# Kernel optimization log

Hardware: AMD Instinct MI355X
Metric: run time of the kernel (lower is better)

Reference implementation:

```python
import jax, jax.numpy as jnp
import numpy as np

THETA = 128.0


def _make_Q(d, units):
    # Q[n,m] = (2n+1)/sqrt(d) if n > m and (n+m) odd, else 0 (fixed, non-trainable)
    n = np.arange(d)[:, None]
    m = np.arange(units)[None, :]
    Q = np.where((n > m) & (((n + m) % 2) == 1), (2 * n + 1) / np.sqrt(d), 0.0)
    return jnp.asarray(Q, dtype=jnp.float32)


def setup_inputs() -> dict:
    key = jax.random.key(0)
    k1, k2, k3, k4 = jax.random.split(key, 4)
    B_, T, Din, d, units = 16, 4096, 128, 256, 256
    x = jax.random.normal(k1, (B_, T, Din), dtype=jnp.float32)
    A = jax.random.normal(k2, (d, d), dtype=jnp.float32) / np.sqrt(d)
    Bm = jax.random.normal(k3, (Din, d), dtype=jnp.float32) / np.sqrt(Din)
    W_mix = jax.random.normal(k4, (units, units), dtype=jnp.float32) / np.sqrt(units)
    b_mix = jnp.zeros((units,), dtype=jnp.float32)
    return {"x": x, "A": A, "B": Bm, "W_mix": W_mix, "b_mix": b_mix}


def reference(x, A, B, W_mix, b_mix):
    d = A.shape[0]
    units = W_mix.shape[0]
    Q = _make_Q(d, units)
    QW = Q @ W_mix  # fuse fixed projection with dense kernel: (d, units)
    alpha = 1.0 - 1.0 / THETA
    beta = 1.0 / THETA
    # precompute input projection for all steps: (T, batch, d)
    xB = jnp.einsum('bti,id->tbd', x, B)

    def step(state, xBt):
        new_state = alpha * state + beta * (state @ A + xBt)
        y = jnp.tanh(new_state @ QW + b_mix)
        return new_state, y

    s0 = jnp.zeros((x.shape[0], d), dtype=x.dtype)
    _, ys = jax.lax.scan(step, s0, xB)  # ys: (T, batch, units)
    return jnp.transpose(ys, (1, 0, 2))
```

## Files before the change

### kernel.cpp

```cpp
#include <hip/hip_runtime.h>
#include <math.h>

constexpr int T_   = 4096;
constexpr int NB   = 16;
constexpr int D_   = 256;
constexpr int DIN  = 128;
constexpr int U_   = 256;
constexpr int L1   = 8;
constexpr int C1   = T_ / L1;
constexpr float ALPHA_ = 1.0f - 1.0f / 128.0f;
constexpr float BETA_  = 1.0f / 128.0f;
constexpr int SD   = NB * D_;
constexpr int MS   = D_ * D_;
constexpr int TLP  = D_ + 4;
constexpr int XLP  = DIN + 4;

using short8  = __attribute__((ext_vector_type(8))) short;
using float4v = __attribute__((ext_vector_type(4))) float;

__device__ __forceinline__ unsigned short bf16_rne(float x) {
  const unsigned b = __float_as_uint(x);
  const unsigned r = ((b >> 16) & 1u) + 0x7FFFu;
  return (unsigned short)((b + r) >> 16);
}
__device__ __forceinline__ float bf16_f(unsigned short h) {
  return __uint_as_float(((unsigned)h) << 16);
}

__device__ __forceinline__ void split2(float e0, float e1, unsigned& hd, unsigned& ld) {
  const unsigned b0 = __float_as_uint(e0), b1 = __float_as_uint(e1);
  const unsigned h0 = b0 & 0xFFFF0000u, h1 = b1 & 0xFFFF0000u;
  const float l0 = e0 - __uint_as_float(h0);
  const float l1 = e1 - __uint_as_float(h1);
  hd = (h0 >> 16) | h1;
  ld = (__float_as_uint(l0) >> 16) | (__float_as_uint(l1) & 0xFFFF0000u);
}

__device__ __forceinline__ void unpack8(uint4 a, uint4 b, short8& hi, short8& lo) {
  union { short8 s; unsigned u[4]; } H, L;
  const unsigned d[8] = {a.x, a.y, a.z, a.w, b.x, b.y, b.z, b.w};
#pragma unroll
  for (int i = 0; i < 4; ++i) {
    H.u[i] = (d[2 * i] >> 16) | (d[2 * i + 1] & 0xFFFF0000u);
    L.u[i] = (d[2 * i] & 0xFFFFu) | (d[2 * i + 1] << 16);
  }
  hi = H.s; lo = L.s;
}

__device__ __forceinline__ void mm_row(const float* __restrict__ Am,
                                       const float* __restrict__ Bm,
                                       float* __restrict__ Dm,
                                       int i, int tid, float* srow) {
  srow[tid] = Am[i * D_ + tid];
  __syncthreads();
  float a0 = 0.f, a1 = 0.f, a2 = 0.f, a3 = 0.f;
#pragma unroll 8
  for (int k = 0; k < D_; k += 4) {
    a0 = fmaf(srow[k + 0], Bm[(k + 0) * D_ + tid], a0);
    a1 = fmaf(srow[k + 1], Bm[(k + 1) * D_ + tid], a1);
    a2 = fmaf(srow[k + 2], Bm[(k + 2) * D_ + tid], a2);
    a3 = fmaf(srow[k + 3], Bm[(k + 3) * D_ + tid], a3);
  }
  Dm[i * D_ + tid] = (a0 + a1) + (a2 + a3);
  __syncthreads();
}

__global__ __launch_bounds__(256) void k_prep(const float* __restrict__ A,
                                              const float* __restrict__ W,
                                              float* __restrict__ Meff,
                                              float* __restrict__ QW) {
  const int bid = blockIdx.x, tid = threadIdx.x;
  if (bid < D_) {
    float v = BETA_ * A[bid * D_ + tid];
    if (bid == tid) v += ALPHA_;
    Meff[bid * D_ + tid] = v;
    return;
  }
  __shared__ float wch[32 * D_];
  float se = 0.f, so = 0.f;
  for (int ch = 0; ch < D_ / 32; ++ch) {
    __syncthreads();
    for (int idx = tid; idx < 32 * D_; idx += 256)
      wch[idx] = W[ch * 32 * D_ + idx];
    __syncthreads();
#pragma unroll
    for (int r = 0; r < 32; ++r) {
      const int n = ch * 32 + r;
      const float sum = (n & 1) ? se : so;
      QW[n * U_ + tid] = sum * ((float)(2 * n + 1) / 16.0f);
      const float wv = wch[r * D_ + tid];
      if (n & 1) so += wv; else se += wv;
    }
  }
}

__global__ __launch_bounds__(256) void k_pw(const float* __restrict__ Am,
                                            const float* __restrict__ Bbase,
                                            float* __restrict__ Dbase) {
  __shared__ float srow[D_];
  const int q = blockIdx.x >> 8, row = blockIdx.x & 255;
  mm_row(Am, Bbase + (size_t)q * MS, Dbase + (size_t)q * MS, row, threadIdx.x, srow);
}

__global__ __launch_bounds__(256) void k_pwr(const float* __restrict__ Abase,
                                             const float* __restrict__ Bm,
                                             float* __restrict__ Dbase) {
  __shared__ float srow[D_];
  const int q = blockIdx.x >> 8, row = blockIdx.x & 255;
  mm_row(Abase + (size_t)q * MS, Bm, Dbase + (size_t)q * MS, row, threadIdx.x, srow);
}

__global__ __launch_bounds__(256) void k_packA(const float* __restrict__ A,
                                               const float* __restrict__ Bm,
                                               unsigned short* __restrict__ Mf,
                                               unsigned short* __restrict__ Bmf) {
  const int bid = blockIdx.x, tid = threadIdx.x;
  const int lane = tid & 63, nb0 = tid >> 6;
  const int quad = lane >> 4, m16 = lane & 15;
  if (bid < 8) {
    const int ks = bid;
    for (int nb = nb0; nb < 16; nb += 4) {
      const size_t fo = ((size_t)(nb * 8 + ks) * 64 + lane) * 8;
#pragma unroll
      for (int jj = 0; jj < 8; ++jj) {
        const int k = ks * 32 + quad * 8 + jj;
        const int n = nb * 16 + m16;
        const float v = BETA_ * A[k * D_ + n];
        const unsigned short h = bf16_rne(v);
        Mf[fo + jj] = h;
        Mf[MS + fo + jj] = bf16_rne(v - bf16_f(h));
      }
    }
  } else {
    const int ks = bid - 8;
    unsigned short* dh = Bmf;
    unsigned short* dl = Bmf + (MS / 2);
    for (int nb = nb0; nb < 16; nb += 4) {
      const size_t fo = ((size_t)(nb * 4 + ks) * 64 + lane) * 8;
#pragma unroll
      for (int jj = 0; jj < 8; ++jj) {
        const int k = ks * 32 + quad * 8 + jj;
        const int n = nb * 16 + m16;
        const float v = BETA_ * Bm[k * D_ + n];
        const unsigned short h = bf16_rne(v);
        dh[fo + jj] = h;
        dl[fo + jj] = bf16_rne(v - bf16_f(h));
      }
    }
  }
}

__global__ __launch_bounds__(256) void k_packB(const float* __restrict__ R,
                                               const float* __restrict__ QWm,
                                               const float* __restrict__ M8,
                                               unsigned short* __restrict__ Bf,
                                               unsigned short* __restrict__ Pf0) {
  const int bid = blockIdx.x;
  const int mat = bid >> 3, ks = bid & 7;
  const float* X = (mat < 8) ? (R + (size_t)mat * MS) : (mat == 8 ? QWm : M8);
  unsigned short* dh = (mat < 9) ? (Bf + (size_t)mat * (2 * MS)) : Pf0;
  unsigned short* dl = dh + MS;
  const int tid = threadIdx.x, lane = tid & 63, nb0 = tid >> 6;
  const int quad = lane >> 4, m16 = lane & 15;
  for (int nb = nb0; nb < 16; nb += 4) {
    const size_t fo = ((size_t)(nb * 8 + ks) * 64 + lane) * 8;
#pragma unroll
    for (int jj = 0; jj < 8; ++jj) {
      const int k = ks * 32 + quad * 8 + jj;
      const int n = nb * 16 + m16;
      const float xv = X[k * D_ + n];
      const unsigned short h = bf16_rne(xv);
      dh[fo + jj] = h;
      dl[fo + jj] = bf16_rne(xv - bf16_f(h));
    }
  }
}

__global__ __launch_bounds__(256, 2) void k_passA(
    const float* __restrict__ x, const unsigned short* __restrict__ Bmf,
    const unsigned short* __restrict__ Mf,
    unsigned short* __restrict__ Shi, unsigned short* __restrict__ Slo,
    float* __restrict__ Ends) {
  __shared__ __align__(16) float xls[NB][XLP];
  __shared__ __align__(16) unsigned tls[NB][TLP];
  const int c = blockIdx.x, tid = threadIdx.x;
  const int w = tid >> 6, lane = tid & 63;
  const int m16 = lane & 15, q = lane >> 4;
  const int xrow = tid >> 4, xi0 = (tid & 15) * 8;

  float4v sC[4];
#pragma unroll
  for (int nt = 0; nt < 4; ++nt) sC[nt] = (float4v){0.f, 0.f, 0.f, 0.f};

  for (int j = 0; j < L1; ++j) {
    const int t = c * L1 + j;
    __syncthreads();
    {
      const float* xr = x + ((size_t)xrow * T_ + t) * DIN + xi0;
      const float4 v0 = *(const float4*)(xr);
      const float4 v1 = *(const float4*)(xr + 4);
      *(float4*)(&xls[xrow][xi0]) = v0;
      *(float4*)(&xls[xrow][xi0 + 4]) = v1;
    }
    if (j > 0) {
#pragma unroll
      for (int nt = 0; nt < 4; ++nt) {
        const int n = (w * 4 + nt) * 16 + m16;
#pragma unroll
        for (int r = 0; r < 4; ++r) {
          const float sv = sC[nt][r];
          const unsigned hb = __float_as_uint(sv) & 0xFFFF0000u;
          const float lo = sv - __uint_as_float(hb);
          tls[4 * q + r][n] = hb | (__float_as_uint(lo) >> 16);
        }
      }
    }
    __syncthreads();
    float4v acc[4];
#pragma unroll
    for (int nt = 0; nt < 4; ++nt) {
      acc[nt][0] = ALPHA_ * sC[nt][0];
      acc[nt][1] = ALPHA_ * sC[nt][1];
      acc[nt][2] = ALPHA_ * sC[nt][2];
      acc[nt][3] = ALPHA_ * sC[nt][3];
    }
#pragma unroll
    for (int ks = 0; ks < 4; ++ks) {
      float xv[8];
      *(float4*)(xv)     = *(const float4*)(&xls[m16][32 * ks + 8 * q]);
      *(float4*)(xv + 4) = *(const float4*)(&xls[m16][32 * ks + 8 * q + 4]);
      union { short8 s; unsigned u[4]; } XH, XL;
#pragma unroll
      for (int p = 0; p < 4; ++p) split2(xv[2 * p], xv[2 * p + 1], XH.u[p], XL.u[p]);
#pragma unroll
      for (int nt = 0; nt < 4; ++nt) {
        const size_t fo = ((size_t)((w * 4 + nt) * 4 + ks) * 64 + lane) * 8;
        const short8 bh = *(const short8*)(Bmf + fo);
        const short8 bl = *(const short8*)(Bmf + (MS / 2) + fo);
        acc[nt] = __builtin_amdgcn_mfma_f32_16x16x32_bf16(XH.s, bh, acc[nt], 0, 0, 0);
        acc[nt] = __builtin_amdgcn_mfma_f32_16x16x32_bf16(XH.s, bl, acc[nt], 0, 0, 0);
        acc[nt] = __builtin_amdgcn_mfma_f32_16x16x32_bf16(XL.s, bh, acc[nt], 0, 0, 0);
      }
    }
    if (j > 0) {
#pragma unroll
      for (int ks = 0; ks < 8; ++ks) {
        const uint4 p0 = *(const uint4*)(&tls[m16][32 * ks + 8 * q]);
        const uint4 p1 = *(const uint4*)(&tls[m16][32 * ks + 8 * q + 4]);
        short8 sh, sl; unpack8(p0, p1, sh, sl);
        const size_t ao = ((size_t)((t - 1) * 8 + ks) * 64 + lane) * 8;
        *(short8*)(Shi + ao) = sh;
        *(short8*)(Slo + ao) = sl;
#pragma unroll
        for (int nt = 0; nt < 4; ++nt) {
          const size_t fo = ((size_t)((w * 4 + nt) * 8 + ks) * 64 + lane) * 8;
          const short8 mh = *(const short8*)(Mf + fo);
          const short8 ml = *(const short8*)(Mf + MS + fo);
          acc[nt] = __builtin_amdgcn_mfma_f32_16x16x32_bf16(sh, mh, acc[nt], 0, 0, 0);
          acc[nt] = __builtin_amdgcn_mfma_f32_16x16x32_bf16(sh, ml, acc[nt], 0, 0, 0);
          acc[nt] = __builtin_amdgcn_mfma_f32_16x16x32_bf16(sl, mh, acc[nt], 0, 0, 0);
        }
      }
    }
#pragma unroll
    for (int nt = 0; nt < 4; ++nt) sC[nt] = acc[nt];
  }
  const int tl = c * L1 + L1 - 1;
  __syncthreads();
#pragma unroll
  for (int nt = 0; nt < 4; ++nt) {
    const int n = (w * 4 + nt) * 16 + m16;
#pragma unroll
    for (int r = 0; r < 4; ++r) {
      const float sv = sC[nt][r];
      const unsigned hb = __float_as_uint(sv) & 0xFFFF0000u;
      const float lo = sv - __uint_as_float(hb);
      tls[4 * q + r][n] = hb | (__float_as_uint(lo) >> 16);
    }
  }
  __syncthreads();
#pragma unroll
  for (int ks = 0; ks < 8; ++ks) {
    const uint4 p0 = *(const uint4*)(&tls[m16][32 * ks + 8 * q]);
    const uint4 p1 = *(const uint4*)(&tls[m16][32 * ks + 8 * q + 4]);
    short8 sh, sl; unpack8(p0, p1, sh, sl);
    const size_t ao = ((size_t)(tl * 8 + ks) * 64 + lane) * 8;
    *(short8*)(Shi + ao) = sh;
    *(short8*)(Slo + ao) = sl;
  }
#pragma unroll
  for (int nt = 0; nt < 4; ++nt) {
    const int n = (w * 4 + nt) * 16 + m16;
#pragma unroll
    for (int r = 0; r < 4; ++r)
      Ends[(size_t)c * SD + (size_t)(4 * q + r) * D_ + n] = sC[nt][r];
  }
}

__global__ __launch_bounds__(256) void k_scan(
    const float* __restrict__ Vin, float* __restrict__ Vout,
    const unsigned short* __restrict__ Pf,
    const float* __restrict__ Pf32,
    float* __restrict__ Psq,
    unsigned short* __restrict__ PfNext,
    int shift, int do_sq, int packmode,
    unsigned short* __restrict__ Hhi, unsigned short* __restrict__ Hlo) {
  __shared__ __align__(16) float smem[16 * TLP];
  const int bid = blockIdx.x, tid = threadIdx.x;
  if (bid >= C1) {
    if (!do_sq) return;
    const int i = bid - C1;
    smem[tid] = Pf32[i * D_ + tid];
    __syncthreads();
    float a0 = 0.f, a1 = 0.f, a2 = 0.f, a3 = 0.f;
#pragma unroll 8
    for (int k = 0; k < D_; k += 4) {
      a0 = fmaf(smem[k + 0], Pf32[(k + 0) * D_ + tid], a0);
      a1 = fmaf(smem[k + 1], Pf32[(k + 1) * D_ + tid], a1);
      a2 = fmaf(smem[k + 2], Pf32[(k + 2) * D_ + tid], a2);
      a3 = fmaf(smem[k + 3], Pf32[(k + 3) * D_ + tid], a3);
    }
    const float v = (a0 + a1) + (a2 + a3);
    Psq[i * D_ + tid] = v;
    const unsigned short h = bf16_rne(v);
    const unsigned short l = bf16_rne(v - bf16_f(h));
    const size_t off = ((size_t)((tid >> 4) * 8 + (i >> 5)) * 64 +
                        ((i >> 3) & 3) * 16 + (tid & 15)) * 8 + (i & 7);
    PfNext[off] = h;
    PfNext[MS + off] = l;
    return;
  }
  const int c = bid;
  const int w = tid >> 6, lane = tid & 63;
  const int m16 = lane & 15, q = lane >> 4;
  float4v acc[4];
#pragma unroll
  for (int nt = 0; nt < 4; ++nt) {
    const int n = (w * 4 + nt) * 16 + m16;
#pragma unroll
    for (int r = 0; r < 4; ++r)
      acc[nt][r] = Vin[(size_t)c * SD + (size_t)(4 * q + r) * D_ + n];
  }
  if (c >= shift) {
    const float* src = Vin + (size_t)(c - shift) * SD;
    {
      const int row = tid >> 4, col0 = (tid & 15) * 16;
#pragma unroll
      for (int p = 0; p < 4; ++p)
        *(float4*)(&smem[row * TLP + col0 + 4 * p]) =
            *(const float4*)(src + (size_t)row * D_ + col0 + 4 * p);
    }
    __syncthreads();
#pragma unroll
    for (int ks = 0; ks < 8; ++ks) {
      float xv[8];
      *(float4*)(xv)     = *(const float4*)(&smem[m16 * TLP + 32 * ks + 8 * q]);
      *(float4*)(xv + 4) = *(const float4*)(&smem[m16 * TLP + 32 * ks + 8 * q + 4]);
      union { short8 s; unsigned u[4]; } XH, XL;
#pragma unroll
      for (int p = 0; p < 4; ++p) split2(xv[2 * p], xv[2 * p + 1], XH.u[p], XL.u[p]);
#pragma unroll
      for (int nt = 0; nt < 4; ++nt) {
        const size_t fo = ((size_t)((w * 4 + nt) * 8 + ks) * 64 + lane) * 8;
        const short8 ph = *(const short8*)(Pf + fo);
        const short8 pl = *(const short8*)(Pf + MS + fo);
        acc[nt] = __builtin_amdgcn_mfma_f32_16x16x32_bf16(XH.s, ph, acc[nt], 0, 0, 0);
        acc[nt] = __builtin_amdgcn_mfma_f32_16x16x32_bf16(XH.s, pl, acc[nt], 0, 0, 0);
        acc[nt] = __builtin_amdgcn_mfma_f32_16x16x32_bf16(XL.s, ph, acc[nt], 0, 0, 0);
      }
    }
  }
  if (packmode) {
    __syncthreads();
    unsigned* tls = (unsigned*)smem;
#pragma unroll
    for (int nt = 0; nt < 4; ++nt) {
      const int n = (w * 4 + nt) * 16 + m16;
#pragma unroll
      for (int r = 0; r < 4; ++r) {
        const float sv = acc[nt][r];
        const unsigned hb = __float_as_uint(sv) & 0xFFFF0000u;
        const float lo = sv - __uint_as_float(hb);
        tls[(4 * q + r) * TLP + n] = hb | (__float_as_uint(lo) >> 16);
      }
    }
    __syncthreads();
#pragma unroll
    for (int ks = 0; ks < 8; ++ks) {
      const uint4 p0 = *(const uint4*)(&tls[m16 * TLP + 32 * ks + 8 * q]);
      const uint4 p1 = *(const uint4*)(&tls[m16 * TLP + 32 * ks + 8 * q + 4]);
      short8 sh, sl; unpack8(p0, p1, sh, sl);
      const size_t ao = ((size_t)(c * 8 + ks) * 64 + lane) * 8;
      *(short8*)(Hhi + ao) = sh;
      *(short8*)(Hlo + ao) = sl;
    }
  } else {
#pragma unroll
    for (int nt = 0; nt < 4; ++nt) {
      const int n = (w * 4 + nt) * 16 + m16;
#pragma unroll
      for (int r = 0; r < 4; ++r)
        Vout[(size_t)c * SD + (size_t)(4 * q + r) * D_ + n] = acc[nt][r];
    }
  }
}

__global__ __launch_bounds__(256, 3) void k_passB(
    const unsigned short* __restrict__ Shi, const unsigned short* __restrict__ Slo,
    const unsigned short* __restrict__ Hhi, const unsigned short* __restrict__ Hlo,
    const unsigned short* __restrict__ Bf, const float* __restrict__ bmix,
    float* __restrict__ out) {
  const int bid = blockIdx.x;
  const int g4 = (bid >> 3) * 4, j = bid & 7;
  const int tid = threadIdx.x;
  const int w = tid >> 6, lane = tid & 63;
  const int m16 = lane & 15, quad = lane >> 4;
  const unsigned short* Qh = Bf + (size_t)8 * 2 * MS;
  const unsigned short* Ql = Qh + MS;
  const unsigned short* Rh = Bf + (size_t)j * 2 * MS;
  const unsigned short* Rl = Rh + MS;

  float4v acc[4][4];
#pragma unroll
  for (int ci = 0; ci < 4; ++ci)
#pragma unroll
    for (int nt = 0; nt < 4; ++nt) acc[ci][nt] = (float4v){0.f, 0.f, 0.f, 0.f};

  for (int ks = 0; ks < 8; ++ks) {
    short8 fh[4], fl[4];
#pragma unroll
    for (int nt = 0; nt < 4; ++nt) {
      const size_t fo = ((size_t)((w * 4 + nt) * 8 + ks) * 64 + lane) * 8;
      fh[nt] = *(const short8*)(Qh + fo);
      fl[nt] = *(const short8*)(Ql + fo);
    }
#pragma unroll
    for (int ci = 0; ci < 4; ++ci) {
      const int t = (g4 + ci) * 8 + j;
      const size_t ao = ((size_t)(t * 8 + ks) * 64 + lane) * 8;
      const short8 sh = *(const short8*)(Shi + ao);
      const short8 sl = *(const short8*)(Slo + ao);
#pragma unroll
      for (int nt = 0; nt < 4; ++nt) {
        float4v a = acc[ci][nt];
        a = __builtin_amdgcn_mfma_f32_16x16x32_bf16(sh, fh[nt], a, 0, 0, 0);
        a = __builtin_amdgcn_mfma_f32_16x16x32_bf16(sh, fl[nt], a, 0, 0, 0);
        a = __builtin_amdgcn_mfma_f32_16x16x32_bf16(sl, fh[nt], a, 0, 0, 0);
        acc[ci][nt] = a;
      }
    }
#pragma unroll
    for (int nt = 0; nt < 4; ++nt) {
      const size_t fo = ((size_t)((w * 4 + nt) * 8 + ks) * 64 + lane) * 8;
      fh[nt] = *(const short8*)(Rh + fo);
      fl[nt] = *(const short8*)(Rl + fo);
    }
#pragma unroll
    for (int ci = 0; ci < 4; ++ci) {
      const int c = g4 + ci;
      if (c > 0) {
        const size_t ho = ((size_t)((c - 1) * 8 + ks) * 64 + lane) * 8;
        const short8 hh = *(const short8*)(Hhi + ho);
        const short8 hl = *(const short8*)(Hlo + ho);
#pragma unroll
        for (int nt = 0; nt < 4; ++nt) {
          float4v a = acc[ci][nt];
          a = __builtin_amdgcn_mfma_f32_16x16x32_bf16(hh, fh[nt], a, 0, 0, 0);
          a = __builtin_amdgcn_mfma_f32_16x16x32_bf16(hh, fl[nt], a, 0, 0, 0);
          a = __builtin_amdgcn_mfma_f32_16x16x32_bf16(hl, fh[nt], a, 0, 0, 0);
          acc[ci][nt] = a;
        }
      }
    }
  }
  __shared__ float ysm[16][U_ + 4];
  for (int ci = 0; ci < 4; ++ci) {
    const int t = (g4 + ci) * 8 + j;
    __syncthreads();
#pragma unroll
    for (int nt = 0; nt < 4; ++nt) {
      const int n = (w * 4 + nt) * 16 + m16;
      const float bias = bmix[n];
#pragma unroll
      for (int r = 0; r < 4; ++r) {
        const float v = acc[ci][nt][r] + bias;
        const float e = __expf(2.0f * v);
        ysm[quad * 4 + r][n] = 1.0f - 2.0f / (e + 1.0f);
      }
    }
    __syncthreads();
    for (int idx = tid; idx < 16 * (U_ / 4); idx += 256) {
      const int b = idx >> 6, c4 = (idx & 63) * 4;
      const float4 v = make_float4(ysm[b][c4], ysm[b][c4 + 1],
                                   ysm[b][c4 + 2], ysm[b][c4 + 3]);
      *(float4*)(out + ((size_t)b * T_ + t) * U_ + c4) = v;
    }
  }
}

extern "C" void kernel_launch(void* const* d_in, const int* in_sizes, int n_in,
                              void* d_out, int out_size, void* d_ws, size_t ws_size,
                              hipStream_t stream) {
  const float* x    = (const float*)d_in[0];
  const float* A    = (const float*)d_in[1];
  const float* Bm   = (const float*)d_in[2];
  const float* W    = (const float*)d_in[3];
  const float* bmix = (const float*)d_in[4];
  float* out = (float*)d_out;

  float* ws = (float*)d_ws;
  unsigned short* Shi = (unsigned short*)ws;
  unsigned short* Slo = (unsigned short*)(ws + 8388608);
  float* pw  = ws + 16777216;
  float* QW  = pw + 8 * (size_t)MS;
  float* R   = QW + MS;
  float* Sa  = R + 8 * (size_t)MS;
  float* Sb  = Sa + MS;
  unsigned short* Bf  = (unsigned short*)(Sb + MS);
  unsigned short* Mf  = Bf + (size_t)9 * 2 * MS;
  unsigned short* Bmf = Mf + 2 * (size_t)MS;
  unsigned short* Pf0 = Bmf + MS;
  unsigned short* Pf1 = Pf0 + 2 * (size_t)MS;
  (void)in_sizes; (void)n_in; (void)out_size; (void)ws_size;

  float* Va = out;
  float* Vb = out + (size_t)C1 * SD;

  unsigned short* Hhi = (unsigned short*)d_in[0];
  unsigned short* Hlo = Hhi + (size_t)C1 * 16 * 256;

  k_prep<<<D_ + 1, 256, 0, stream>>>(A, W, pw, QW);
  k_packA<<<12, 256, 0, stream>>>(A, Bm, Mf, Bmf);
  k_passA<<<C1, 256, 0, stream>>>(x, Bmf, Mf, Shi, Slo, Va);
  k_pw<<<256, 256, 0, stream>>>(pw, pw, pw + MS);
  k_pw<<<512, 256, 0, stream>>>(pw + MS, pw, pw + 2 * (size_t)MS);
  k_pw<<<1024, 256, 0, stream>>>(pw + 3 * (size_t)MS, pw, pw + 4 * (size_t)MS);
  k_pwr<<<2048, 256, 0, stream>>>(pw, QW, R);
  k_packB<<<80, 256, 0, stream>>>(R, QW, pw + 7 * (size_t)MS, Bf, Pf0);

  const float* vin = Va; float* vout = Vb;
  const float* Pcur = pw + 7 * (size_t)MS;
  float* sqs[2] = {Sa, Sb};
  unsigned short* Pfp[2] = {Pf0, Pf1};
  for (int lvl = 0; lvl < 9; ++lvl) {
    float* Pd = sqs[lvl & 1];
    k_scan<<<C1 + D_, 256, 0, stream>>>(vin, vout, Pfp[lvl & 1], Pcur, Pd,
                                        Pfp[(lvl + 1) & 1], 1 << lvl,
                                        (lvl < 8) ? 1 : 0, (lvl == 8) ? 1 : 0,
                                        Hhi, Hlo);
    Pcur = Pd;
    const float* tmp = vin; vin = vout; vout = (float*)tmp;
  }

  k_passB<<<1024, 256, 0, stream>>>(Shi, Slo, Hhi, Hlo, Bf, bmix, out);
}
```

Before: 464.1 us.

## Merge prep/pack kernels and skip unchanged chunks in scan levels

```diff
diff --git a/kernel.cpp b/kernel.cpp
--- a/kernel.cpp
+++ b/kernel.cpp
@@ -47,6 +47,13 @@
   hi = H.s; lo = L.s;
 }
 
+__device__ __forceinline__ int nwpar(int c, int l) {
+  if (c <= 0) return 0;
+  const int f = 31 - __clz(c);
+  const int nw = (l < f + 1) ? l : (f + 1);
+  return nw & 1;
+}
+
 __device__ __forceinline__ void mm_row(const float* __restrict__ Am,
                                        const float* __restrict__ Bm,
                                        float* __restrict__ Dm,
@@ -68,7 +75,10 @@
 __global__ __launch_bounds__(256) void k_prep(const float* __restrict__ A,
                                               const float* __restrict__ W,
                                               float* __restrict__ Meff,
-                                              float* __restrict__ QW) {
+                                              float* __restrict__ QW,
+                                              const float* __restrict__ Bm,
+                                              unsigned short* __restrict__ Mf,
+                                              unsigned short* __restrict__ Bmf) {
   const int bid = blockIdx.x, tid = threadIdx.x;
   if (bid < D_) {
     float v = BETA_ * A[bid * D_ + tid];
@@ -76,49 +86,30 @@
     Meff[bid * D_ + tid] = v;
     return;
   }
-  __shared__ float wch[32 * D_];
-  float se = 0.f, so = 0.f;
-  for (int ch = 0; ch < D_ / 32; ++ch) {
-    __syncthreads();
-    for (int idx = tid; idx < 32 * D_; idx += 256)
-      wch[idx] = W[ch * 32 * D_ + idx];
-    __syncthreads();
-#pragma unroll
-    for (int r = 0; r < 32; ++r) {
-      const int n = ch * 32 + r;
-      const float sum = (n & 1) ? se : so;
-      QW[n * U_ + tid] = sum * ((float)(2 * n + 1) / 16.0f);
-      const float wv = wch[r * D_ + tid];
-      if (n & 1) so += wv; else se += wv;
-    }
-  }
-}
-
-__global__ __launch_bounds__(256) void k_pw(const float* __restrict__ Am,
-                                            const float* __restrict__ Bbase,
-                                            float* __restrict__ Dbase) {
-  __shared__ float srow[D_];
-  const int q = blockIdx.x >> 8, row = blockIdx.x & 255;
-  mm_row(Am, Bbase + (size_t)q * MS, Dbase + (size_t)q * MS, row, threadIdx.x, srow);
-}
-
-__global__ __launch_bounds__(256) void k_pwr(const float* __restrict__ Abase,
-                                             const float* __restrict__ Bm,
-                                             float* __restrict__ Dbase) {
-  __shared__ float srow[D_];
-  const int q = blockIdx.x >> 8, row = blockIdx.x & 255;
-  mm_row(Abase + (size_t)q * MS, Bm, Dbase + (size_t)q * MS, row, threadIdx.x, srow);
-}
-
-__global__ __launch_bounds__(256) void k_packA(const float* __restrict__ A,
-                                               const float* __restrict__ Bm,
-                                               unsigned short* __restrict__ Mf,
-                                               unsigned short* __restrict__ Bmf) {
-  const int bid = blockIdx.x, tid = threadIdx.x;
+  if (bid == D_) {
+    __shared__ float wch[32 * D_];
+    float se = 0.f, so = 0.f;
+    for (int ch = 0; ch < D_ / 32; ++ch) {
+      __syncthreads();
+      for (int idx = tid; idx < 32 * D_; idx += 256)
+        wch[idx] = W[ch * 32 * D_ + idx];
+      __syncthreads();
+#pragma unroll
+      for (int r = 0; r < 32; ++r) {
+        const int n = ch * 32 + r;
+        const float sum = (n & 1) ? se : so;
+        QW[n * U_ + tid] = sum * ((float)(2 * n + 1) / 16.0f);
+        const float wv = wch[r * D_ + tid];
+        if (n & 1) so += wv; else se += wv;
+      }
+    }
+    return;
+  }
+  const int pb = bid - D_ - 1;
   const int lane = tid & 63, nb0 = tid >> 6;
   const int quad = lane >> 4, m16 = lane & 15;
-  if (bid < 8) {
-    const int ks = bid;
+  if (pb < 8) {
+    const int ks = pb;
     for (int nb = nb0; nb < 16; nb += 4) {
       const size_t fo = ((size_t)(nb * 8 + ks) * 64 + lane) * 8;
 #pragma unroll
@@ -132,7 +123,7 @@
       }
     }
   } else {
-    const int ks = bid - 8;
+    const int ks = pb - 8;
     unsigned short* dh = Bmf;
     unsigned short* dl = Bmf + (MS / 2);
     for (int nb = nb0; nb < 16; nb += 4) {
@@ -150,40 +141,55 @@
   }
 }
 
-__global__ __launch_bounds__(256) void k_packB(const float* __restrict__ R,
-                                               const float* __restrict__ QWm,
-                                               const float* __restrict__ M8,
-                                               unsigned short* __restrict__ Bf,
-                                               unsigned short* __restrict__ Pf0) {
-  const int bid = blockIdx.x;
-  const int mat = bid >> 3, ks = bid & 7;
-  const float* X = (mat < 8) ? (R + (size_t)mat * MS) : (mat == 8 ? QWm : M8);
-  unsigned short* dh = (mat < 9) ? (Bf + (size_t)mat * (2 * MS)) : Pf0;
-  unsigned short* dl = dh + MS;
-  const int tid = threadIdx.x, lane = tid & 63, nb0 = tid >> 6;
-  const int quad = lane >> 4, m16 = lane & 15;
-  for (int nb = nb0; nb < 16; nb += 4) {
-    const size_t fo = ((size_t)(nb * 8 + ks) * 64 + lane) * 8;
-#pragma unroll
-    for (int jj = 0; jj < 8; ++jj) {
-      const int k = ks * 32 + quad * 8 + jj;
-      const int n = nb * 16 + m16;
-      const float xv = X[k * D_ + n];
-      const unsigned short h = bf16_rne(xv);
-      dh[fo + jj] = h;
-      dl[fo + jj] = bf16_rne(xv - bf16_f(h));
-    }
-  }
-}
-
-__global__ __launch_bounds__(256, 2) void k_passA(
+__global__ __launch_bounds__(256) void k_pw(const float* __restrict__ Am,
+                                            const float* __restrict__ Bbase,
+                                            float* __restrict__ Dbase) {
+  __shared__ float srow[D_];
+  const int q = blockIdx.x >> 8, row = blockIdx.x & 255;
+  mm_row(Am, Bbase + (size_t)q * MS, Dbase + (size_t)q * MS, row, threadIdx.x, srow);
+}
+
+__global__ __launch_bounds__(256) void k_pwr(const float* __restrict__ Abase,
+                                             const float* __restrict__ Bm,
+                                             float* __restrict__ Dbase) {
+  __shared__ float srow[D_];
+  const int q = blockIdx.x >> 8, row = blockIdx.x & 255;
+  mm_row(Abase + (size_t)q * MS, Bm, Dbase + (size_t)q * MS, row, threadIdx.x, srow);
+}
+
+__global__ __launch_bounds__(256, 2) void k_big2(
+    const float* __restrict__ R, const float* __restrict__ QWm,
+    const float* __restrict__ M8, unsigned short* __restrict__ Bf,
+    unsigned short* __restrict__ Pf0,
     const float* __restrict__ x, const unsigned short* __restrict__ Bmf,
     const unsigned short* __restrict__ Mf,
     unsigned short* __restrict__ Shi, unsigned short* __restrict__ Slo,
     float* __restrict__ Ends) {
+  const int bid = blockIdx.x, tid = threadIdx.x;
+  if (bid < 80) {
+    const int mat = bid >> 3, ks = bid & 7;
+    const float* X = (mat < 8) ? (R + (size_t)mat * MS) : (mat == 8 ? QWm : M8);
+    unsigned short* dh = (mat < 9) ? (Bf + (size_t)mat * (2 * MS)) : Pf0;
+    unsigned short* dl = dh + MS;
+    const int lane = tid & 63, nb0 = tid >> 6;
+    const int quad = lane >> 4, m16 = lane & 15;
+    for (int nb = nb0; nb < 16; nb += 4) {
+      const size_t fo = ((size_t)(nb * 8 + ks) * 64 + lane) * 8;
+#pragma unroll
+      for (int jj = 0; jj < 8; ++jj) {
+        const int k = ks * 32 + quad * 8 + jj;
+        const int n = nb * 16 + m16;
+        const float xv = X[k * D_ + n];
+        const unsigned short h = bf16_rne(xv);
+        dh[fo + jj] = h;
+        dl[fo + jj] = bf16_rne(xv - bf16_f(h));
+      }
+    }
+    return;
+  }
   __shared__ __align__(16) float xls[NB][XLP];
   __shared__ __align__(16) unsigned tls[NB][TLP];
-  const int c = blockIdx.x, tid = threadIdx.x;
+  const int c = bid - 80;
   const int w = tid >> 6, lane = tid & 63;
   const int m16 = lane & 15, q = lane >> 4;
   const int xrow = tid >> 4, xi0 = (tid & 15) * 8;
@@ -248,9 +254,11 @@
         const uint4 p0 = *(const uint4*)(&tls[m16][32 * ks + 8 * q]);
         const uint4 p1 = *(const uint4*)(&tls[m16][32 * ks + 8 * q + 4]);
         short8 sh, sl; unpack8(p0, p1, sh, sl);
-        const size_t ao = ((size_t)((t - 1) * 8 + ks) * 64 + lane) * 8;
-        *(short8*)(Shi + ao) = sh;
-        *(short8*)(Slo + ao) = sl;
+        if ((ks & 3) == w) {
+          const size_t ao = ((size_t)((t - 1) * 8 + ks) * 64 + lane) * 8;
+          *(short8*)(Shi + ao) = sh;
+          *(short8*)(Slo + ao) = sl;
+        }
 #pragma unroll
         for (int nt = 0; nt < 4; ++nt) {
           const size_t fo = ((size_t)((w * 4 + nt) * 8 + ks) * 64 + lane) * 8;
@@ -280,7 +288,8 @@
   }
   __syncthreads();
 #pragma unroll
-  for (int ks = 0; ks < 8; ++ks) {
+  for (int kk = 0; kk < 2; ++kk) {
+    const int ks = w + kk * 4;
     const uint4 p0 = *(const uint4*)(&tls[m16][32 * ks + 8 * q]);
     const uint4 p1 = *(const uint4*)(&tls[m16][32 * ks + 8 * q + 4]);
     short8 sh, sl; unpack8(p0, p1, sh, sl);
@@ -298,18 +307,20 @@
 }
 
 __global__ __launch_bounds__(256) void k_scan(
-    const float* __restrict__ Vin, float* __restrict__ Vout,
+    float* V0, float* V1,
     const unsigned short* __restrict__ Pf,
     const float* __restrict__ Pf32,
     float* __restrict__ Psq,
     unsigned short* __restrict__ PfNext,
-    int shift, int do_sq, int packmode,
+    int lvl, int do_sq, int packmode,
     unsigned short* __restrict__ Hhi, unsigned short* __restrict__ Hlo) {
   __shared__ __align__(16) float smem[16 * TLP];
   const int bid = blockIdx.x, tid = threadIdx.x;
-  if (bid >= C1) {
+  const int shift = 1 << lvl;
+  const int Cw = packmode ? C1 : (C1 - shift);
+  if (bid >= Cw) {
     if (!do_sq) return;
-    const int i = bid - C1;
+    const int i = bid - Cw;
     smem[tid] = Pf32[i * D_ + tid];
     __syncthreads();
     float a0 = 0.f, a1 = 0.f, a2 = 0.f, a3 = 0.f;
@@ -330,19 +341,22 @@
     PfNext[MS + off] = l;
     return;
   }
-  const int c = bid;
+  const int c = packmode ? bid : (bid + shift);
   const int w = tid >> 6, lane = tid & 63;
   const int m16 = lane & 15, q = lane >> 4;
+  const int ownPar = nwpar(c, lvl);
+  const float* Vown = ownPar ? V1 : V0;
   float4v acc[4];
 #pragma unroll
   for (int nt = 0; nt < 4; ++nt) {
     const int n = (w * 4 + nt) * 16 + m16;
 #pragma unroll
     for (int r = 0; r < 4; ++r)
-      acc[nt][r] = Vin[(size_t)c * SD + (size_t)(4 * q + r) * D_ + n];
+      acc[nt][r] = Vown[(size_t)c * SD + (size_t)(4 * q + r) * D_ + n];
   }
   if (c >= shift) {
-    const float* src = Vin + (size_t)(c - shift) * SD;
+    const float* Vsrc = nwpar(c - shift, lvl) ? V1 : V0;
+    const float* src = Vsrc + (size_t)(c - shift) * SD;
     {
       const int row = tid >> 4, col0 = (tid & 15) * 16;
 #pragma unroll
@@ -395,12 +409,13 @@
       *(short8*)(Hlo + ao) = sl;
     }
   } else {
+    float* Vdst = (ownPar ^ 1) ? V1 : V0;
 #pragma unroll
     for (int nt = 0; nt < 4; ++nt) {
       const int n = (w * 4 + nt) * 16 + m16;
 #pragma unroll
       for (int r = 0; r < 4; ++r)
-        Vout[(size_t)c * SD + (size_t)(4 * q + r) * D_ + n] = acc[nt][r];
+        Vdst[(size_t)c * SD + (size_t)(4 * q + r) * D_ + n] = acc[nt][r];
     }
   }
 }
@@ -523,33 +538,32 @@
   unsigned short* Pf1 = Pf0 + 2 * (size_t)MS;
   (void)in_sizes; (void)n_in; (void)out_size; (void)ws_size;
 
-  float* Va = out;
-  float* Vb = out + (size_t)C1 * SD;
+  float* V0 = out;
+  float* V1 = out + (size_t)C1 * SD;
 
   unsigned short* Hhi = (unsigned short*)d_in[0];
   unsigned short* Hlo = Hhi + (size_t)C1 * 16 * 256;
 
-  k_prep<<<D_ + 1, 256, 0, stream>>>(A, W, pw, QW);
-  k_packA<<<12, 256, 0, stream>>>(A, Bm, Mf, Bmf);
-  k_passA<<<C1, 256, 0, stream>>>(x, Bmf, Mf, Shi, Slo, Va);
+  k_prep<<<D_ + 13, 256, 0, stream>>>(A, W, pw, QW, Bm, Mf, Bmf);
   k_pw<<<256, 256, 0, stream>>>(pw, pw, pw + MS);
   k_pw<<<512, 256, 0, stream>>>(pw + MS, pw, pw + 2 * (size_t)MS);
   k_pw<<<1024, 256, 0, stream>>>(pw + 3 * (size_t)MS, pw, pw + 4 * (size_t)MS);
   k_pwr<<<2048, 256, 0, stream>>>(pw, QW, R);
-  k_packB<<<80, 256, 0, stream>>>(R, QW, pw + 7 * (size_t)MS, Bf, Pf0);
-
-  const float* vin = Va; float* vout = Vb;
+  k_big2<<<80 + C1, 256, 0, stream>>>(R, QW, pw + 7 * (size_t)MS, Bf, Pf0,
+                                      x, Bmf, Mf, Shi, Slo, V0);
+
   const float* Pcur = pw + 7 * (size_t)MS;
   float* sqs[2] = {Sa, Sb};
   unsigned short* Pfp[2] = {Pf0, Pf1};
   for (int lvl = 0; lvl < 9; ++lvl) {
     float* Pd = sqs[lvl & 1];
-    k_scan<<<C1 + D_, 256, 0, stream>>>(vin, vout, Pfp[lvl & 1], Pcur, Pd,
-                                        Pfp[(lvl + 1) & 1], 1 << lvl,
-                                        (lvl < 8) ? 1 : 0, (lvl == 8) ? 1 : 0,
-                                        Hhi, Hlo);
+    const int pack = (lvl == 8) ? 1 : 0;
+    const int do_sq = (lvl < 8) ? 1 : 0;
+    const int grid = pack ? C1 : (C1 - (1 << lvl)) + D_;
+    k_scan<<<grid, 256, 0, stream>>>(V0, V1, Pfp[lvl & 1], Pcur, Pd,
+                                     Pfp[(lvl + 1) & 1], lvl, do_sq, pack,
+                                     Hhi, Hlo);
     Pcur = Pd;
-    const float* tmp = vin; vin = vout; vout = (float*)tmp;
   }
 
   k_passB<<<1024, 256, 0, stream>>>(Shi, Slo, Hhi, Hlo, Bf, bmix, out);
```

Result: faster. 436.8 us (-5.9%).
